# Kernel optimization log

Measured on AMD Instinct MI355X. Metric: run time of the kernel, lower is better.

Reference implementation:

```python
import jax, jax.numpy as jnp
import numpy as np

B, C, T, W, H = 32, 80, 2048, 128, 512
FRAMES_PER_WORD = T // W  # 16
K = 5  # conv kernel size (Component approximated as Conv1d(k=5)+ReLU)


def conv1d(x, w, b):
    # x: [B, Cin, T], w: [Cout, Cin, K] -> [B, Cout, T] (SAME padding)
    y = jax.lax.conv_general_dilated(
        x, w, window_strides=(1,), padding='SAME',
        dimension_numbers=('NCH', 'OIH', 'NCH'))
    return y + b[None, :, None]


def setup_inputs() -> dict:
    key = jax.random.key(0)
    k1, k2, k3 = jax.random.split(key, 3)
    features = jax.random.normal(k1, (B, C, T), dtype=jnp.float32)
    # word bounds: contiguous equal-length spans [start, end) covering all T frames
    starts = (jnp.arange(W, dtype=jnp.int64) * FRAMES_PER_WORD)
    ends = starts + FRAMES_PER_WORD
    word_bounds = jnp.broadcast_to(jnp.stack([starts, ends])[None], (B, 2, W))
    word_lengths = jnp.full((B,), W, dtype=jnp.int64)
    enc_w = jax.random.normal(k2, (H, C, K), dtype=jnp.float32) * 0.02
    enc_b = jnp.zeros((H,), dtype=jnp.float32)
    dec_w = jax.random.normal(k3, (1, H, K), dtype=jnp.float32) * 0.02
    dec_b = jnp.zeros((1,), dtype=jnp.float32)
    return {'features': features, 'word_bounds': word_bounds,
            'word_lengths': word_lengths, 'enc_w': enc_w, 'enc_b': enc_b,
            'dec_w': dec_w, 'dec_b': dec_b}


def reference(features, word_bounds, word_lengths, enc_w, enc_b, dec_w, dec_b):
    # Frame encoder: Conv1d + ReLU -> [B, H, T]
    frame_embedding = jax.nn.relu(conv1d(features, enc_w, enc_b))
    t = jnp.arange(T)
    start = word_bounds[:, 0, :]  # [B, W]
    end = word_bounds[:, 1, :]    # [B, W]
    # Ragged per-word mean pooling, fused as a masked matmul (segment mean).
    mask = (t[None, None, :] >= start[..., None]) & (t[None, None, :] < end[..., None])  # [B, W, T]
    valid = jnp.arange(W)[None, :] < word_lengths[:, None]  # [B, W]
    maskf = (mask & valid[..., None]).astype(frame_embedding.dtype)
    counts = jnp.maximum(maskf.sum(-1), 1.0)  # [B, W]
    word_embeddings = jnp.einsum('bct,bwt->bcw', frame_embedding, maskf) / counts[:, None, :]
    # Word decoder: Conv1d over the word axis -> [B, 1, W]
    return conv1d(word_embeddings, dec_w, dec_b)
```

## Files before the change

kernel.cpp:

```cpp
#include <hip/hip_runtime.h>

#define B_ 32
#define C_ 80
#define T_ 2048
#define W_ 128
#define H_ 512
#define K_ 5

#define KTOT 400
#define KPAD 416
#define NKI  13
#define TM   128
#define TN   128
#define SF_STRIDE 88
#define SF_ROWS   136
#define BF_ELEMS  (4 * NKI * 2 * 4 * 64 * 8)

typedef _Float16 half8 __attribute__((ext_vector_type(8)));
typedef float    f4v   __attribute__((ext_vector_type(4)));

__global__ __launch_bounds__(256) void convert_feat(const float* __restrict__ feat,
                                                    _Float16* __restrict__ featT) {
    __shared__ _Float16 tile[64 * 80];
    const int bid = blockIdx.x;
    const int b = bid >> 5, tc = bid & 31;
    const int t0 = tc * 64;
    for (int idx = threadIdx.x; idx < 80 * 64; idx += 256) {
        int cc = idx >> 6, tt = idx & 63;
        float v = feat[((size_t)b * C_ + cc) * T_ + t0 + tt];
        tile[tt * 80 + cc] = (_Float16)v;
    }
    __syncthreads();
    for (int idx = threadIdx.x; idx < 64 * 10; idx += 256) {
        int tt = idx / 10, g = idx % 10;
        *(f4v*)(featT + ((size_t)b * T_ + t0 + tt) * C_ + g * 8) =
            *(const f4v*)(tile + tt * 80 + g * 8);
    }
}

__global__ void make_bfrag(const float* __restrict__ enc_w,
                           _Float16* __restrict__ Bf) {
    int idx = blockIdx.x * 256 + threadIdx.x;
    if (idx >= BF_ELEMS) return;
    int e  = idx & 7;
    int l  = (idx >> 3) & 63;
    int j  = (idx >> 9) & 3;
    int w2 = (idx >> 11) & 1;
    int it = (idx >> 12) % NKI;
    int nt = idx / (NKI << 12);
    int h  = nt * 128 + w2 * 64 + j * 16 + (l & 15);
    int kc = it * 32 + (l >> 4) * 8 + e;
    float v = 0.f;
    if (kc < KTOT) v = enc_w[(h * C_ + kc % 80) * K_ + kc / 80];
    Bf[idx] = (_Float16)v;
}

__global__ __launch_bounds__(256) void prep_words3(const int* __restrict__ bounds,
                                                   const int* __restrict__ lengths,
                                                   int* __restrict__ word_of,
                                                   float* __restrict__ inv_cnt) {
    const int b = blockIdx.x;
    const int tid = threadIdx.x;
    int* wob = word_of + b * T_;
    for (int t = tid; t < T_; t += 256) wob[t] = -1;
    __syncthreads();
    if (tid < W_) {
        const int len = lengths[b];
        int s = bounds[(b * 2 + 0) * W_ + tid];
        int e = bounds[(b * 2 + 1) * W_ + tid];
        s = max(s, 0); e = min(e, T_);
        bool valid = (tid < len) && (e > s);
        inv_cnt[b * W_ + tid] = valid ? 1.f / (float)(e - s) : 0.f;
        if (valid)
            for (int t = s; t < e; ++t) wob[t] = tid;
    }
}

__global__ __launch_bounds__(256) void gemm_enc(
    const _Float16* __restrict__ featT,
    const _Float16* __restrict__ Bf,
    const float*    __restrict__ enc_b,
    const int*      __restrict__ word_of,
    const float*    __restrict__ inv_cnt,
    float*          __restrict__ wemb)
{
    __shared__ _Float16 sf[SF_ROWS * SF_STRIDE];

    const int tid = threadIdx.x;
    const int bid = blockIdx.x;
    const int nt = bid & 3;
    const int mt = (bid >> 2) & 15;
    const int b  = bid >> 6;
    const int t0 = mt * TM;
    const int h0 = nt * TN;

    const _Float16* fb = featT + (size_t)b * T_ * C_;
    for (int idx = tid; idx < SF_ROWS * 10; idx += 256) {
        int tt = idx / 10, g = idx % 10;
        int t = t0 - 2 + tt;
        int tcl = min(max(t, 0), T_ - 1);
        f4v v = {};
        if (t >= 0 && t < T_) v = *(const f4v*)(fb + tcl * C_ + g * 8);
        *(f4v*)(sf + tt * SF_STRIDE + g * 8) = v;
    }

    const int lane = tid & 63;
    const int wid  = tid >> 6;
    const int wm = (wid >> 1) * 64;
    const int wn = (wid & 1) * 64;
    const int w2 = wid & 1;
    const int ml = lane & 15;
    const int q  = lane >> 4;

    const half8* bfp = (const half8*)(Bf + (((nt * NKI) * 2 + w2) * 4 * 64 + lane) * 8);

    f4v acc[4][4] = {};

    __syncthreads();

    int c = q * 8;
    int aoff = (wm + ml) * SF_STRIDE + c;

    half8 bcur[4];
    #pragma unroll
    for (int j = 0; j < 4; ++j) bcur[j] = bfp[j * 64];

    for (int it = 0; it < NKI; ++it) {
        half8 bnext[4];
        if (it + 1 < NKI) {
            const half8* bn = bfp + (it + 1) * (2 * 4 * 64);
            #pragma unroll
            for (int j = 0; j < 4; ++j) bnext[j] = bn[j * 64];
        }
        half8 af[4];
        #pragma unroll
        for (int i = 0; i < 4; ++i)
            af[i] = *(const half8*)(sf + aoff + i * 16 * SF_STRIDE);
        #pragma unroll
        for (int i = 0; i < 4; ++i)
            #pragma unroll
            for (int j = 0; j < 4; ++j)
                acc[i][j] = __builtin_amdgcn_mfma_f32_16x16x32_f16(af[i], bcur[j], acc[i][j], 0, 0, 0);
        #pragma unroll
        for (int j = 0; j < 4; ++j) bcur[j] = bnext[j];
        aoff += 32; c += 32;
        if (c >= 80) { c -= 80; aoff += 8; }
    }

    const int bT = b * T_;
    const int bW = b * W_;
    float bias[4];
    #pragma unroll
    for (int j = 0; j < 4; ++j) bias[j] = enc_b[h0 + wn + j * 16 + ml];

    #pragma unroll
    for (int i = 0; i < 4; ++i) {
        const int tg = t0 + wm + i * 16;
        const int w0  = word_of[bT + tg];
        const int w15 = word_of[bT + tg + 15];
        if (w0 == w15) {
            if (w0 >= 0) {
                const float inv = inv_cnt[bW + w0];
                const bool own_lo = (tg == 0) || (word_of[bT + tg - 1] != w0);
                const bool own_hi = (tg + 16 >= T_) || (word_of[bT + tg + 16] != w0);
                #pragma unroll
                for (int j = 0; j < 4; ++j) {
                    float s = 0.f;
                    #pragma unroll
                    for (int r = 0; r < 4; ++r) s += fmaxf(acc[i][j][r] + bias[j], 0.f);
                    s += __shfl_down(s, 32, 64);
                    s += __shfl_down(s, 16, 64);
                    if (q == 0) {
                        float val = s * inv;
                        float* dst = &wemb[(size_t)(bW + w0) * H_ + h0 + wn + j * 16 + ml];
                        if (own_lo && own_hi) *dst = val;
                        else atomicAdd(dst, val);
                    }
                }
            }
        } else {
            #pragma unroll
            for (int j = 0; j < 4; ++j) {
                #pragma unroll
                for (int r = 0; r < 4; ++r) {
                    int t = tg + q * 4 + r;
                    int w = word_of[bT + t];
                    if (w >= 0)
                        atomicAdd(&wemb[(size_t)(bW + w) * H_ + h0 + wn + j * 16 + ml],
                                  fmaxf(acc[i][j][r] + bias[j], 0.f) * inv_cnt[bW + w]);
                }
            }
        }
    }
}

__global__ __launch_bounds__(256) void dec_e(const float* __restrict__ wemb,
                                             const float* __restrict__ dec_w,
                                             float* __restrict__ e) {
    __shared__ float sdw[H_ * K_];
    for (int idx = threadIdx.x; idx < H_ * K_; idx += 256) sdw[idx] = dec_w[idx];
    __syncthreads();
    const int pair = blockIdx.x * 4 + (threadIdx.x >> 6);
    const int lane = threadIdx.x & 63;
    const float* row = wemb + (size_t)pair * H_;
    float a[K_] = {};
    #pragma unroll
    for (int hh = 0; hh < H_ / 64; ++hh) {
        int h = hh * 64 + lane;
        float v = row[h];
        #pragma unroll
        for (int k = 0; k < K_; ++k) a[k] += v * sdw[h * K_ + k];
    }
    #pragma unroll
    for (int k = 0; k < K_; ++k) {
        #pragma unroll
        for (int off = 32; off > 0; off >>= 1) a[k] += __shfl_down(a[k], off, 64);
    }
    if (lane == 0) {
        #pragma unroll
        for (int k = 0; k < K_; ++k) e[pair * K_ + k] = a[k];
    }
}

__global__ void dec_combine(const float* __restrict__ e,
                            const float* __restrict__ dec_b,
                            float* __restrict__ out) {
    int idx = blockIdx.x * 256 + threadIdx.x;
    if (idx >= B_ * W_) return;
    int b = idx >> 7, w = idx & 127;
    float acc = dec_b[0];
    #pragma unroll
    for (int k = 0; k < K_; ++k) {
        int wq = w + k - 2;
        if (wq >= 0 && wq < W_) acc += e[(b * W_ + wq) * K_ + k];
    }
    out[idx] = acc;
}

extern "C" void kernel_launch(void* const* d_in, const int* in_sizes, int n_in,
                              void* d_out, int out_size, void* d_ws, size_t ws_size,
                              hipStream_t stream) {
    const float* feat    = (const float*)d_in[0];
    const int*   bounds  = (const int*)  d_in[1];
    const int*   lengths = (const int*)  d_in[2];
    const float* enc_w   = (const float*)d_in[3];
    const float* enc_b   = (const float*)d_in[4];
    const float* dec_w   = (const float*)d_in[5];
    const float* dec_b   = (const float*)d_in[6];
    float* out = (float*)d_out;

    char* p = (char*)d_ws;
    _Float16* featT = (_Float16*)p;  p += (size_t)B_ * T_ * C_ * 2;
    _Float16* Bf    = (_Float16*)p;  p += (size_t)BF_ELEMS * 2;
    int* word_of    = (int*)p;       p += (size_t)B_ * T_ * 4;
    float* inv_cnt  = (float*)p;     p += (size_t)B_ * W_ * 4;
    float* wemb     = (float*)p;     p += (size_t)B_ * W_ * H_ * 4;
    float* evec     = (float*)p;

    hipMemsetAsync(wemb, 0, (size_t)B_ * W_ * H_ * 4, stream);

    convert_feat<<<B_ * (T_ / 64), 256, 0, stream>>>(feat, featT);
    make_bfrag<<<(BF_ELEMS + 255) / 256, 256, 0, stream>>>(enc_w, Bf);
    prep_words3<<<B_, 256, 0, stream>>>(bounds, lengths, word_of, inv_cnt);
    gemm_enc<<<B_ * (T_ / TM) * (H_ / TN), 256, 0, stream>>>(featT, Bf, enc_b,
                                                             word_of, inv_cnt, wemb);
    dec_e<<<B_ * W_ / 4, 256, 0, stream>>>(wemb, dec_w, evec);
    dec_combine<<<(B_ * W_ + 255) / 256, 256, 0, stream>>>(evec, dec_b, out);
}
```

Baseline: 132.9 us.

## Fuse decoder conv into encoder GEMM epilogue and merge prep kernels

The word-decoder convolution is folded into the GEMM epilogue. Each block projects its pooled partial word embeddings onto the decoder weights, accumulates per-word taps in shared memory, and atomically adds the results into the output. This removes the full word-embedding buffer, its memset, and the two decoder kernels. The four preparation kernels are also merged into one launch that initializes the output with the bias. The cost is extra shared-memory atomics and global atomics on the output, which also makes the floating-point summation order nondeterministic.

```diff
diff --git a/kernel.cpp b/kernel.cpp
--- a/kernel.cpp
+++ b/kernel.cpp
@@ -16,75 +16,86 @@
 #define SF_ROWS   136
 #define BF_ELEMS  (4 * NKI * 2 * 4 * 64 * 8)
 
+#define RB_FEAT   1024
+#define RB_BFRAG  (RB_FEAT + BF_ELEMS / 256)
+#define RB_WORDS  (RB_BFRAG + B_)
+#define RB_OUT    (RB_WORDS + (B_ * W_) / 256)
+
 typedef _Float16 half8 __attribute__((ext_vector_type(8)));
 typedef float    f4v   __attribute__((ext_vector_type(4)));
 
-__global__ __launch_bounds__(256) void convert_feat(const float* __restrict__ feat,
-                                                    _Float16* __restrict__ featT) {
+__global__ __launch_bounds__(256) void prep_all(
+    const float* __restrict__ feat, const float* __restrict__ enc_w,
+    const int* __restrict__ bounds, const int* __restrict__ lengths,
+    const float* __restrict__ dec_b,
+    _Float16* __restrict__ featT, _Float16* __restrict__ Bf,
+    int* __restrict__ word_of, float* __restrict__ inv_cnt,
+    float* __restrict__ out)
+{
     __shared__ _Float16 tile[64 * 80];
     const int bid = blockIdx.x;
-    const int b = bid >> 5, tc = bid & 31;
-    const int t0 = tc * 64;
-    for (int idx = threadIdx.x; idx < 80 * 64; idx += 256) {
-        int cc = idx >> 6, tt = idx & 63;
-        float v = feat[((size_t)b * C_ + cc) * T_ + t0 + tt];
-        tile[tt * 80 + cc] = (_Float16)v;
-    }
-    __syncthreads();
-    for (int idx = threadIdx.x; idx < 64 * 10; idx += 256) {
-        int tt = idx / 10, g = idx % 10;
-        *(f4v*)(featT + ((size_t)b * T_ + t0 + tt) * C_ + g * 8) =
-            *(const f4v*)(tile + tt * 80 + g * 8);
+    const int tid = threadIdx.x;
+
+    if (bid < RB_FEAT) {
+        const int b = bid >> 5, tc = bid & 31;
+        const int t0 = tc * 64;
+        for (int idx = tid; idx < 80 * 64; idx += 256) {
+            int cc = idx >> 6, tt = idx & 63;
+            float v = feat[((size_t)b * C_ + cc) * T_ + t0 + tt];
+            tile[tt * 80 + cc] = (_Float16)v;
+        }
+        __syncthreads();
+        for (int idx = tid; idx < 64 * 10; idx += 256) {
+            int tt = idx / 10, g = idx % 10;
+            *(f4v*)(featT + ((size_t)b * T_ + t0 + tt) * C_ + g * 8) =
+                *(const f4v*)(tile + tt * 80 + g * 8);
+        }
+    } else if (bid < RB_BFRAG) {
+        int idx = (bid - RB_FEAT) * 256 + tid;
+        int e  = idx & 7;
+        int l  = (idx >> 3) & 63;
+        int j  = (idx >> 9) & 3;
+        int w2 = (idx >> 11) & 1;
+        int it = (idx >> 12) % NKI;
+        int nt = idx / (NKI << 12);
+        int h  = nt * 128 + w2 * 64 + j * 16 + (l & 15);
+        int kc = it * 32 + (l >> 4) * 8 + e;
+        float v = 0.f;
+        if (kc < KTOT) v = enc_w[(h * C_ + kc % 80) * K_ + kc / 80];
+        Bf[idx] = (_Float16)v;
+    } else if (bid < RB_WORDS) {
+        const int b = bid - RB_BFRAG;
+        int* wob = word_of + b * T_;
+        for (int t = tid; t < T_; t += 256) wob[t] = -1;
+        __syncthreads();
+        if (tid < W_) {
+            const int len = lengths[b];
+            int s = bounds[(b * 2 + 0) * W_ + tid];
+            int e = bounds[(b * 2 + 1) * W_ + tid];
+            s = max(s, 0); e = min(e, T_);
+            bool valid = (tid < len) && (e > s);
+            inv_cnt[b * W_ + tid] = valid ? 1.f / (float)(e - s) : 0.f;
+            if (valid)
+                for (int t = s; t < e; ++t) wob[t] = tid;
+        }
+    } else {
+        int idx = (bid - RB_WORDS) * 256 + tid;
+        if (idx < B_ * W_) out[idx] = dec_b[0];
     }
 }
 
-__global__ void make_bfrag(const float* __restrict__ enc_w,
-                           _Float16* __restrict__ Bf) {
-    int idx = blockIdx.x * 256 + threadIdx.x;
-    if (idx >= BF_ELEMS) return;
-    int e  = idx & 7;
-    int l  = (idx >> 3) & 63;
-    int j  = (idx >> 9) & 3;
-    int w2 = (idx >> 11) & 1;
-    int it = (idx >> 12) % NKI;
-    int nt = idx / (NKI << 12);
-    int h  = nt * 128 + w2 * 64 + j * 16 + (l & 15);
-    int kc = it * 32 + (l >> 4) * 8 + e;
-    float v = 0.f;
-    if (kc < KTOT) v = enc_w[(h * C_ + kc % 80) * K_ + kc / 80];
-    Bf[idx] = (_Float16)v;
-}
-
-__global__ __launch_bounds__(256) void prep_words3(const int* __restrict__ bounds,
-                                                   const int* __restrict__ lengths,
-                                                   int* __restrict__ word_of,
-                                                   float* __restrict__ inv_cnt) {
-    const int b = blockIdx.x;
-    const int tid = threadIdx.x;
-    int* wob = word_of + b * T_;
-    for (int t = tid; t < T_; t += 256) wob[t] = -1;
-    __syncthreads();
-    if (tid < W_) {
-        const int len = lengths[b];
-        int s = bounds[(b * 2 + 0) * W_ + tid];
-        int e = bounds[(b * 2 + 1) * W_ + tid];
-        s = max(s, 0); e = min(e, T_);
-        bool valid = (tid < len) && (e > s);
-        inv_cnt[b * W_ + tid] = valid ? 1.f / (float)(e - s) : 0.f;
-        if (valid)
-            for (int t = s; t < e; ++t) wob[t] = tid;
-    }
-}
-
-__global__ __launch_bounds__(256) void gemm_enc(
+__global__ __launch_bounds__(256) void gemm_enc_fused(
     const _Float16* __restrict__ featT,
     const _Float16* __restrict__ Bf,
     const float*    __restrict__ enc_b,
     const int*      __restrict__ word_of,
     const float*    __restrict__ inv_cnt,
-    float*          __restrict__ wemb)
+    const float*    __restrict__ dec_w,
+    float*          __restrict__ out)
 {
     __shared__ _Float16 sf[SF_ROWS * SF_STRIDE];
+    __shared__ float    sdw[TN * K_];
+    __shared__ float    eloc[W_ + 4];
 
     const int tid = threadIdx.x;
     const int bid = blockIdx.x;
@@ -103,6 +114,8 @@
         if (t >= 0 && t < T_) v = *(const f4v*)(fb + tcl * C_ + g * 8);
         *(f4v*)(sf + tt * SF_STRIDE + g * 8) = v;
     }
+    for (int idx = tid; idx < TN * K_; idx += 256) sdw[idx] = dec_w[h0 * K_ + idx];
+    if (tid < W_ + 4) eloc[tid] = 0.f;
 
     const int lane = tid & 63;
     const int wid  = tid >> 6;
@@ -161,8 +174,6 @@
         if (w0 == w15) {
             if (w0 >= 0) {
                 const float inv = inv_cnt[bW + w0];
-                const bool own_lo = (tg == 0) || (word_of[bT + tg - 1] != w0);
-                const bool own_hi = (tg + 16 >= T_) || (word_of[bT + tg + 16] != w0);
                 #pragma unroll
                 for (int j = 0; j < 4; ++j) {
                     float s = 0.f;
@@ -171,70 +182,45 @@
                     s += __shfl_down(s, 32, 64);
                     s += __shfl_down(s, 16, 64);
                     if (q == 0) {
-                        float val = s * inv;
-                        float* dst = &wemb[(size_t)(bW + w0) * H_ + h0 + wn + j * 16 + ml];
-                        if (own_lo && own_hi) *dst = val;
-                        else atomicAdd(dst, val);
+                        const float val = s * inv;
+                        const int hl = (wn + j * 16 + ml) * K_;
+                        #pragma unroll
+                        for (int k = 0; k < K_; ++k) {
+                            float p = val * sdw[hl + k];
+                            p += __shfl_xor(p, 1, 64);
+                            p += __shfl_xor(p, 2, 64);
+                            p += __shfl_xor(p, 4, 64);
+                            p += __shfl_xor(p, 8, 64);
+                            if (ml == 0) atomicAdd(&eloc[w0 + 4 - k], p);
+                        }
                     }
                 }
             }
         } else {
             #pragma unroll
             for (int j = 0; j < 4; ++j) {
+                const int hl = (wn + j * 16 + ml) * K_;
                 #pragma unroll
                 for (int r = 0; r < 4; ++r) {
                     int t = tg + q * 4 + r;
                     int w = word_of[bT + t];
-                    if (w >= 0)
-                        atomicAdd(&wemb[(size_t)(bW + w) * H_ + h0 + wn + j * 16 + ml],
-                                  fmaxf(acc[i][j][r] + bias[j], 0.f) * inv_cnt[bW + w]);
+                    if (w >= 0) {
+                        float val = fmaxf(acc[i][j][r] + bias[j], 0.f) * inv_cnt[bW + w];
+                        #pragma unroll
+                        for (int k = 0; k < K_; ++k)
+                            atomicAdd(&eloc[w + 4 - k], val * sdw[hl + k]);
+                    }
                 }
             }
         }
     }
-}
-
-__global__ __launch_bounds__(256) void dec_e(const float* __restrict__ wemb,
-                                             const float* __restrict__ dec_w,
-                                             float* __restrict__ e) {
-    __shared__ float sdw[H_ * K_];
-    for (int idx = threadIdx.x; idx < H_ * K_; idx += 256) sdw[idx] = dec_w[idx];
+
     __syncthreads();
-    const int pair = blockIdx.x * 4 + (threadIdx.x >> 6);
-    const int lane = threadIdx.x & 63;
-    const float* row = wemb + (size_t)pair * H_;
-    float a[K_] = {};
-    #pragma unroll
-    for (int hh = 0; hh < H_ / 64; ++hh) {
-        int h = hh * 64 + lane;
-        float v = row[h];
-        #pragma unroll
-        for (int k = 0; k < K_; ++k) a[k] += v * sdw[h * K_ + k];
-    }
-    #pragma unroll
-    for (int k = 0; k < K_; ++k) {
-        #pragma unroll
-        for (int off = 32; off > 0; off >>= 1) a[k] += __shfl_down(a[k], off, 64);
-    }
-    if (lane == 0) {
-        #pragma unroll
-        for (int k = 0; k < K_; ++k) e[pair * K_ + k] = a[k];
-    }
-}
-
-__global__ void dec_combine(const float* __restrict__ e,
-                            const float* __restrict__ dec_b,
-                            float* __restrict__ out) {
-    int idx = blockIdx.x * 256 + threadIdx.x;
-    if (idx >= B_ * W_) return;
-    int b = idx >> 7, w = idx & 127;
-    float acc = dec_b[0];
-    #pragma unroll
-    for (int k = 0; k < K_; ++k) {
-        int wq = w + k - 2;
-        if (wq >= 0 && wq < W_) acc += e[(b * W_ + wq) * K_ + k];
-    }
-    out[idx] = acc;
+    for (int idx = tid; idx < W_ + 4; idx += 256) {
+        float v = eloc[idx];
+        int w = idx - 2;
+        if (v != 0.f && w >= 0 && w < W_) atomicAdd(&out[bW + w], v);
+    }
 }
 
 extern "C" void kernel_launch(void* const* d_in, const int* in_sizes, int n_in,
@@ -253,17 +239,10 @@
     _Float16* featT = (_Float16*)p;  p += (size_t)B_ * T_ * C_ * 2;
     _Float16* Bf    = (_Float16*)p;  p += (size_t)BF_ELEMS * 2;
     int* word_of    = (int*)p;       p += (size_t)B_ * T_ * 4;
-    float* inv_cnt  = (float*)p;     p += (size_t)B_ * W_ * 4;
-    float* wemb     = (float*)p;     p += (size_t)B_ * W_ * H_ * 4;
-    float* evec     = (float*)p;
-
-    hipMemsetAsync(wemb, 0, (size_t)B_ * W_ * H_ * 4, stream);
-
-    convert_feat<<<B_ * (T_ / 64), 256, 0, stream>>>(feat, featT);
-    make_bfrag<<<(BF_ELEMS + 255) / 256, 256, 0, stream>>>(enc_w, Bf);
-    prep_words3<<<B_, 256, 0, stream>>>(bounds, lengths, word_of, inv_cnt);
-    gemm_enc<<<B_ * (T_ / TM) * (H_ / TN), 256, 0, stream>>>(featT, Bf, enc_b,
-                                                             word_of, inv_cnt, wemb);
-    dec_e<<<B_ * W_ / 4, 256, 0, stream>>>(wemb, dec_w, evec);
-    dec_combine<<<(B_ * W_ + 255) / 256, 256, 0, stream>>>(evec, dec_b, out);
+    float* inv_cnt  = (float*)p;
+
+    prep_all<<<RB_OUT, 256, 0, stream>>>(feat, enc_w, bounds, lengths, dec_b,
+                                         featT, Bf, word_of, inv_cnt, out);
+    gemm_enc_fused<<<B_ * (T_ / TM) * (H_ / TN), 256, 0, stream>>>(
+        featT, Bf, enc_b, word_of, inv_cnt, dec_w, out);
 }
```

Result: slower. 151.3 us (+13.9%).

## Merge prep kernels and memset into one launch, fuse decoder stages

Applied to the files above, without the earlier changes.

Folds the feature transpose, weight fragment packing, word-map preparation and the zeroing of the word-embedding buffer into one block-partitioned prep kernel. The two decoder kernels become a single kernel that computes per-word dot products for a 36-row halo window in shared memory and applies the 5-tap combine in place. The GEMM loop drops its last-iteration guard by padding the fragment buffer one iteration past the end, and gets a launch-bounds occupancy hint of 3. Together these cut launch count and one intermediate buffer, at the cost of recomputing halo rows in the decoder and possible register pressure from the occupancy hint.

```diff
diff --git a/kernel.cpp b/kernel.cpp
--- a/kernel.cpp
+++ b/kernel.cpp
@@ -14,69 +14,78 @@
 #define TN   128
 #define SF_STRIDE 88
 #define SF_ROWS   136
-#define BF_ELEMS  (4 * NKI * 2 * 4 * 64 * 8)
+#define ITER_STRIDE (2 * 4 * 64 * 8)
+#define BF_ELEMS  (4 * NKI * ITER_STRIDE)
+
+#define RB_FEAT   1024
+#define RB_BFRAG  (RB_FEAT + BF_ELEMS / 256)
+#define RB_WORDS  (RB_BFRAG + B_)
+#define RB_WZERO  (RB_WORDS + 128)
 
 typedef _Float16 half8 __attribute__((ext_vector_type(8)));
 typedef float    f4v   __attribute__((ext_vector_type(4)));
 
-__global__ __launch_bounds__(256) void convert_feat(const float* __restrict__ feat,
-                                                    _Float16* __restrict__ featT) {
+__global__ __launch_bounds__(256) void prep_all(
+    const float* __restrict__ feat, const float* __restrict__ enc_w,
+    const int* __restrict__ bounds, const int* __restrict__ lengths,
+    _Float16* __restrict__ featT, _Float16* __restrict__ Bf,
+    int* __restrict__ word_of, float* __restrict__ inv_cnt,
+    float* __restrict__ wemb)
+{
     __shared__ _Float16 tile[64 * 80];
     const int bid = blockIdx.x;
-    const int b = bid >> 5, tc = bid & 31;
-    const int t0 = tc * 64;
-    for (int idx = threadIdx.x; idx < 80 * 64; idx += 256) {
-        int cc = idx >> 6, tt = idx & 63;
-        float v = feat[((size_t)b * C_ + cc) * T_ + t0 + tt];
-        tile[tt * 80 + cc] = (_Float16)v;
-    }
-    __syncthreads();
-    for (int idx = threadIdx.x; idx < 64 * 10; idx += 256) {
-        int tt = idx / 10, g = idx % 10;
-        *(f4v*)(featT + ((size_t)b * T_ + t0 + tt) * C_ + g * 8) =
-            *(const f4v*)(tile + tt * 80 + g * 8);
-    }
-}
-
-__global__ void make_bfrag(const float* __restrict__ enc_w,
-                           _Float16* __restrict__ Bf) {
-    int idx = blockIdx.x * 256 + threadIdx.x;
-    if (idx >= BF_ELEMS) return;
-    int e  = idx & 7;
-    int l  = (idx >> 3) & 63;
-    int j  = (idx >> 9) & 3;
-    int w2 = (idx >> 11) & 1;
-    int it = (idx >> 12) % NKI;
-    int nt = idx / (NKI << 12);
-    int h  = nt * 128 + w2 * 64 + j * 16 + (l & 15);
-    int kc = it * 32 + (l >> 4) * 8 + e;
-    float v = 0.f;
-    if (kc < KTOT) v = enc_w[(h * C_ + kc % 80) * K_ + kc / 80];
-    Bf[idx] = (_Float16)v;
-}
-
-__global__ __launch_bounds__(256) void prep_words3(const int* __restrict__ bounds,
-                                                   const int* __restrict__ lengths,
-                                                   int* __restrict__ word_of,
-                                                   float* __restrict__ inv_cnt) {
-    const int b = blockIdx.x;
     const int tid = threadIdx.x;
-    int* wob = word_of + b * T_;
-    for (int t = tid; t < T_; t += 256) wob[t] = -1;
-    __syncthreads();
-    if (tid < W_) {
-        const int len = lengths[b];
-        int s = bounds[(b * 2 + 0) * W_ + tid];
-        int e = bounds[(b * 2 + 1) * W_ + tid];
-        s = max(s, 0); e = min(e, T_);
-        bool valid = (tid < len) && (e > s);
-        inv_cnt[b * W_ + tid] = valid ? 1.f / (float)(e - s) : 0.f;
-        if (valid)
-            for (int t = s; t < e; ++t) wob[t] = tid;
-    }
-}
-
-__global__ __launch_bounds__(256) void gemm_enc(
+
+    if (bid < RB_FEAT) {
+        const int b = bid >> 5, tc = bid & 31;
+        const int t0 = tc * 64;
+        for (int idx = tid; idx < 80 * 64; idx += 256) {
+            int cc = idx >> 6, tt = idx & 63;
+            float v = feat[((size_t)b * C_ + cc) * T_ + t0 + tt];
+            tile[tt * 80 + cc] = (_Float16)v;
+        }
+        __syncthreads();
+        for (int idx = tid; idx < 64 * 10; idx += 256) {
+            int tt = idx / 10, g = idx % 10;
+            *(f4v*)(featT + ((size_t)b * T_ + t0 + tt) * C_ + g * 8) =
+                *(const f4v*)(tile + tt * 80 + g * 8);
+        }
+    } else if (bid < RB_BFRAG) {
+        int idx = (bid - RB_FEAT) * 256 + tid;
+        int e  = idx & 7;
+        int l  = (idx >> 3) & 63;
+        int j  = (idx >> 9) & 3;
+        int w2 = (idx >> 11) & 1;
+        int it = (idx >> 12) % NKI;
+        int nt = idx / (NKI << 12);
+        int h  = nt * 128 + w2 * 64 + j * 16 + (l & 15);
+        int kc = it * 32 + (l >> 4) * 8 + e;
+        float v = 0.f;
+        if (kc < KTOT) v = enc_w[(h * C_ + kc % 80) * K_ + kc / 80];
+        Bf[idx] = (_Float16)v;
+    } else if (bid < RB_WORDS) {
+        const int b = bid - RB_BFRAG;
+        int* wob = word_of + b * T_;
+        for (int t = tid; t < T_; t += 256) wob[t] = -1;
+        __syncthreads();
+        if (tid < W_) {
+            const int len = lengths[b];
+            int s = bounds[(b * 2 + 0) * W_ + tid];
+            int e = bounds[(b * 2 + 1) * W_ + tid];
+            s = max(s, 0); e = min(e, T_);
+            bool valid = (tid < len) && (e > s);
+            inv_cnt[b * W_ + tid] = valid ? 1.f / (float)(e - s) : 0.f;
+            if (valid)
+                for (int t = s; t < e; ++t) wob[t] = tid;
+        }
+    } else {
+        f4v* wz = (f4v*)wemb;
+        int base = (bid - RB_WORDS) * 256 + tid;
+        for (int i = base; i < (B_ * W_ * H_) / 4; i += 128 * 256) wz[i] = (f4v){};
+    }
+}
+
+__global__ __launch_bounds__(256, 3) void gemm_enc(
     const _Float16* __restrict__ featT,
     const _Float16* __restrict__ Bf,
     const float*    __restrict__ enc_b,
@@ -127,7 +136,7 @@
 
     for (int it = 0; it < NKI; ++it) {
         half8 bnext[4];
-        if (it + 1 < NKI) {
+        {
             const half8* bn = bfp + (it + 1) * (2 * 4 * 64);
             #pragma unroll
             for (int j = 0; j < 4; ++j) bnext[j] = bn[j * 64];
@@ -194,47 +203,49 @@
     }
 }
 
-__global__ __launch_bounds__(256) void dec_e(const float* __restrict__ wemb,
-                                             const float* __restrict__ dec_w,
-                                             float* __restrict__ e) {
+__global__ __launch_bounds__(256) void dec_all(const float* __restrict__ wemb,
+                                               const float* __restrict__ dec_w,
+                                               const float* __restrict__ dec_b,
+                                               float* __restrict__ out) {
     __shared__ float sdw[H_ * K_];
+    __shared__ float se[36][8];
+    const int bid = blockIdx.x;
+    const int b = bid >> 2, ch = bid & 3;
+    const int w0 = ch * 32;
     for (int idx = threadIdx.x; idx < H_ * K_; idx += 256) sdw[idx] = dec_w[idx];
     __syncthreads();
-    const int pair = blockIdx.x * 4 + (threadIdx.x >> 6);
-    const int lane = threadIdx.x & 63;
-    const float* row = wemb + (size_t)pair * H_;
-    float a[K_] = {};
-    #pragma unroll
-    for (int hh = 0; hh < H_ / 64; ++hh) {
-        int h = hh * 64 + lane;
-        float v = row[h];
-        #pragma unroll
-        for (int k = 0; k < K_; ++k) a[k] += v * sdw[h * K_ + k];
-    }
-    #pragma unroll
-    for (int k = 0; k < K_; ++k) {
-        #pragma unroll
-        for (int off = 32; off > 0; off >>= 1) a[k] += __shfl_down(a[k], off, 64);
-    }
-    if (lane == 0) {
-        #pragma unroll
-        for (int k = 0; k < K_; ++k) e[pair * K_ + k] = a[k];
-    }
-}
-
-__global__ void dec_combine(const float* __restrict__ e,
-                            const float* __restrict__ dec_b,
-                            float* __restrict__ out) {
-    int idx = blockIdx.x * 256 + threadIdx.x;
-    if (idx >= B_ * W_) return;
-    int b = idx >> 7, w = idx & 127;
-    float acc = dec_b[0];
-    #pragma unroll
-    for (int k = 0; k < K_; ++k) {
-        int wq = w + k - 2;
-        if (wq >= 0 && wq < W_) acc += e[(b * W_ + wq) * K_ + k];
-    }
-    out[idx] = acc;
+    const int wid = threadIdx.x >> 6, lane = threadIdx.x & 63;
+    for (int row = wid; row < 36; row += 4) {
+        int wq = w0 - 2 + row;
+        float a[K_] = {};
+        if (wq >= 0 && wq < W_) {
+            const float* src = wemb + ((size_t)b * W_ + wq) * H_;
+            #pragma unroll
+            for (int r = 0; r < H_ / 64; ++r) {
+                int h = r * 64 + lane;
+                float v = src[h];
+                #pragma unroll
+                for (int k = 0; k < K_; ++k) a[k] += v * sdw[h * K_ + k];
+            }
+        }
+        #pragma unroll
+        for (int k = 0; k < K_; ++k) {
+            #pragma unroll
+            for (int off = 32; off > 0; off >>= 1) a[k] += __shfl_down(a[k], off, 64);
+        }
+        if (lane == 0) {
+            #pragma unroll
+            for (int k = 0; k < K_; ++k) se[row][k] = a[k];
+        }
+    }
+    __syncthreads();
+    if (threadIdx.x < 32) {
+        int wl = threadIdx.x;
+        float acc = dec_b[0];
+        #pragma unroll
+        for (int k = 0; k < K_; ++k) acc += se[wl + k][k];
+        out[b * W_ + w0 + wl] = acc;
+    }
 }
 
 extern "C" void kernel_launch(void* const* d_in, const int* in_sizes, int n_in,
@@ -251,19 +262,14 @@
 
     char* p = (char*)d_ws;
     _Float16* featT = (_Float16*)p;  p += (size_t)B_ * T_ * C_ * 2;
-    _Float16* Bf    = (_Float16*)p;  p += (size_t)BF_ELEMS * 2;
+    _Float16* Bf    = (_Float16*)p;  p += (size_t)(BF_ELEMS + ITER_STRIDE) * 2;
     int* word_of    = (int*)p;       p += (size_t)B_ * T_ * 4;
     float* inv_cnt  = (float*)p;     p += (size_t)B_ * W_ * 4;
-    float* wemb     = (float*)p;     p += (size_t)B_ * W_ * H_ * 4;
-    float* evec     = (float*)p;
-
-    hipMemsetAsync(wemb, 0, (size_t)B_ * W_ * H_ * 4, stream);
-
-    convert_feat<<<B_ * (T_ / 64), 256, 0, stream>>>(feat, featT);
-    make_bfrag<<<(BF_ELEMS + 255) / 256, 256, 0, stream>>>(enc_w, Bf);
-    prep_words3<<<B_, 256, 0, stream>>>(bounds, lengths, word_of, inv_cnt);
-    gemm_enc<<<B_ * (T_ / TM) * (H_ / TN), 256, 0, stream>>>(featT, Bf, enc_b,
-                                                             word_of, inv_cnt, wemb);
-    dec_e<<<B_ * W_ / 4, 256, 0, stream>>>(wemb, dec_w, evec);
-    dec_combine<<<(B_ * W_ + 255) / 256, 256, 0, stream>>>(evec, dec_b, out);
-}
+    float* wemb     = (float*)p;
+
+    prep_all<<<RB_WZERO, 256, 0, stream>>>(feat, enc_w, bounds, lengths,
+                                           featT, Bf, word_of, inv_cnt, wemb);
+    gemm_enc<<<B_ * (T_ / TM) * (H_ / TN), 256, 0, stream>>>(
+        featT, Bf, enc_b, word_of, inv_cnt, wemb);
+    dec_all<<<B_ * 4, 256, 0, stream>>>(wemb, dec_w, dec_b, out);
+}
```

After: 130.0 us. 2.1% less time.
